# Optimization experiments

Measured on AMD Instinct MI355X. Metric: run time of the kernel, lower is better.

Reference implementation:

```python
import jax, jax.numpy as jnp
import numpy as np

N_NODES = 100000
N_EDGES = 800000
DIM = 128
BN_EPS = 1e-5


def setup_inputs() -> dict:
    key = jax.random.key(0)
    k1, k2, k3 = jax.random.split(key, 3)
    x = jax.random.normal(k1, (N_NODES, DIM), dtype=jnp.float32)
    edge_index = jax.random.randint(k2, (2, N_EDGES), 0, N_NODES, dtype=jnp.int64)
    # xavier-uniform-like init for the linear weight [out, in]
    limit = float(np.sqrt(6.0 / (DIM + DIM)))
    W = jax.random.uniform(k3, (DIM, DIM), dtype=jnp.float32, minval=-limit, maxval=limit)
    bias = jnp.zeros((DIM,), dtype=jnp.float32)
    bn_gamma = jnp.ones((DIM,), dtype=jnp.float32)
    bn_beta = jnp.zeros((DIM,), dtype=jnp.float32)
    return {"x": x, "edge_index": edge_index, "W": W, "bias": bias,
            "bn_gamma": bn_gamma, "bn_beta": bn_beta, "bit_sum": 0}


def reference(x, edge_index, W, bias, bn_gamma, bn_beta, bit_sum):
    n = x.shape[0]
    # Linear (no bias), is_q=False path; q_xw treated as identity.
    h = x @ W.T                                   # [N, D]
    row, col = edge_index[0], edge_index[1]
    # symmetric degree normalization: deg computed over destination (col)
    deg = jax.ops.segment_sum(jnp.ones_like(col, dtype=h.dtype), col, num_segments=n)
    deg_inv_sqrt = jnp.where(deg > 0, jax.lax.rsqrt(jnp.maximum(deg, 1.0)), 0.0)
    norm = deg_inv_sqrt[row] * deg_inv_sqrt[col]  # [E]
    # message: norm * x_j (x_j = h[row]), aggregate (add) at col
    msg = norm[:, None] * h[row]                  # [E, D]
    out = jax.ops.segment_sum(msg, col, num_segments=n)  # [N, D]
    out = out + bias
    # BatchNorm1d (training mode: batch stats, biased variance)
    mean = jnp.mean(out, axis=0)
    var = jnp.var(out, axis=0)
    out = (out - mean) * jax.lax.rsqrt(var + BN_EPS) * bn_gamma + bn_beta
    # activation
    out = jax.nn.relu(out)
    # residual (in_dim == out_dim); dropout p=0 -> identity
    out = out + x
    return (out, 0)
```

## Files before the change

### kernel.cpp

```cpp
#include <hip/hip_runtime.h>
#include <cstddef>

#define NN 100000
#define DD 128
#define ND (NN * DD)
#define BN_EPS 1e-5f
#define LDA 136
#define NREP 16
#define NBKT 392
#define BSH 8
#define EPB 4096
#define NT ((NN + 63) / 64)

typedef __bf16 bf16_t;
typedef bf16_t bf16x8 __attribute__((ext_vector_type(8)));
typedef float f32x4 __attribute__((ext_vector_type(4)));
typedef unsigned int uint;
typedef unsigned short ushort;


__device__ __forceinline__ ushort f2b(float f) {
    uint u = __builtin_bit_cast(uint, f);
    u += 0x7FFFu + ((u >> 16) & 1u);
    return (ushort)(u >> 16);
}
__device__ __forceinline__ float b2f(uint s) {
    return __builtin_bit_cast(float, s << 16);
}
__device__ __forceinline__ float blo(uint u) {
    return __builtin_bit_cast(float, u << 16);
}
__device__ __forceinline__ float bhi(uint u) {
    return __builtin_bit_cast(float, u & 0xFFFF0000u);
}

__device__ __forceinline__ int detect_i64(const int* __restrict__ ei) {
    __shared__ int sflag;
    int t = threadIdx.x;
    if (t < 64) {
        int hi = ei[2 * t + 1];
        unsigned long long b = __ballot(hi == 0);
        if (t == 0) sflag = (b == ~0ull) ? 1 : 0;
    }
    __syncthreads();
    return sflag;
}

__global__ __launch_bounds__(256) void k_prep(const int* __restrict__ ei,
                                              int* __restrict__ bktot, int E, int nbh,
                                              const float* __restrict__ x,
                                              uint* __restrict__ xb,
                                              const float* __restrict__ W,
                                              uint* __restrict__ wb) {
    if ((int)blockIdx.x < nbh) {
        int f = detect_i64(ei);
        __shared__ int hist[NBKT];
        int t = threadIdx.x;
        for (int i = t; i < NBKT; i += 256) hist[i] = 0;
        __syncthreads();
        int base = blockIdx.x * EPB;
        int count = min(EPB, E - base);
        for (int i = t; i < count; i += 256) {
            int e = base + i;
            int c = f ? ei[2 * (E + e)] : ei[E + e];
            atomicAdd(&hist[c >> BSH], 1);
        }
        __syncthreads();
        for (int i = t; i < NBKT; i += 256)
            if (hist[i] > 0) atomicAdd(&bktot[i], hist[i]);
        return;
    }
    int i = (blockIdx.x - nbh) * 256 + threadIdx.x;
    const float* src;
    uint* dst;
    int j;
    if (i < ND / 8) { src = x; dst = xb; j = i; }
    else { j = i - ND / 8; if (j >= (DD * DD) / 8) return; src = W; dst = wb; }
    const float4* s4 = (const float4*)src;
    float4 a = s4[2 * j], b = s4[2 * j + 1];
    uint4 o;
    o.x = (uint)f2b(a.x) | ((uint)f2b(a.y) << 16);
    o.y = (uint)f2b(a.z) | ((uint)f2b(a.w) << 16);
    o.z = (uint)f2b(b.x) | ((uint)f2b(b.y) << 16);
    o.w = (uint)f2b(b.z) | ((uint)f2b(b.w) << 16);
    ((uint4*)dst)[j] = o;
}

__global__ __launch_bounds__(256) void k_bin(const int* __restrict__ ei,
                                             const int* __restrict__ bktot,
                                             int* __restrict__ bcur,
                                             uint2* __restrict__ pairs, int E) {
    int f = detect_i64(ei);
    __shared__ int bb[NBKT], hist[NBKT], scur[NBKT];
    int t = threadIdx.x;
    for (int i = t; i < NBKT; i += 256) { bb[i] = bktot[i]; hist[i] = 0; }
    __syncthreads();
    if (t == 0) {
        int run = 0;
        for (int i = 0; i < NBKT; ++i) { int v = bb[i]; bb[i] = run; run += v; }
    }
    int base = blockIdx.x * EPB;
    int count = min(EPB, E - base);
    int rr[16], cc[16];
#pragma unroll
    for (int k = 0; k < 16; ++k) {
        int i = t + k * 256;
        if (i < count) {
            int e = base + i;
            int r, c;
            if (f) { r = ei[2 * e]; c = ei[2 * (E + e)]; }
            else   { r = ei[e];     c = ei[E + e]; }
            rr[k] = r; cc[k] = c;
            atomicAdd(&hist[c >> BSH], 1);
        }
    }
    __syncthreads();
    for (int i = t; i < NBKT; i += 256)
        if (hist[i] > 0) scur[i] = bb[i] + atomicAdd(&bcur[i], hist[i]);
    __syncthreads();
#pragma unroll
    for (int k = 0; k < 16; ++k) {
        int i = t + k * 256;
        if (i < count) {
            int b = cc[k] >> BSH;
            int pos = atomicAdd(&scur[b], 1);
            pairs[pos] = (uint2){(uint)rr[k], (uint)cc[k]};
        }
    }
}

__global__ __launch_bounds__(256) void k_cnt(const uint2* __restrict__ pairs,
                                             const int* __restrict__ bktot,
                                             int* __restrict__ ptr0,
                                             int* __restrict__ cnt,
                                             float* __restrict__ dinv,
                                             int* __restrict__ srow) {
    __shared__ int sbt[NBKT];
    __shared__ int hist[256], scur[256], ls[256];
    __shared__ int se0, se1;
    int b = blockIdx.x;
    int t = threadIdx.x;
    for (int i = t; i < NBKT; i += 256) sbt[i] = bktot[i];
    hist[t] = 0;
    __syncthreads();
    if (t == 0) {
        int run = 0;
        for (int i = 0; i < b; ++i) run += sbt[i];
        se0 = run; se1 = run + sbt[b];
    }
    __syncthreads();
    int e0 = se0, e1 = se1;
    int nodebase = b << BSH;
    for (int i = e0 + t; i < e1; i += 256)
        atomicAdd(&hist[(int)pairs[i].y - nodebase], 1);
    __syncthreads();
    int c1 = hist[t];
    ls[t] = c1;
    __syncthreads();
    for (int o = 1; o < 256; o <<= 1) {
        int v = (t >= o) ? ls[t - o] : 0;
        __syncthreads();
        ls[t] += v;
        __syncthreads();
    }
    int run = ls[t] - c1 + e0;
    int idx = nodebase + t;
    if (idx < NN) {
        ptr0[idx] = run;
        cnt[idx] = c1;
        dinv[idx] = c1 > 0 ? rsqrtf((float)c1) : 0.f;
    }
    scur[t] = run;
    __syncthreads();
    for (int i = e0 + t; i < e1; i += 256) {
        uint2 p = pairs[i];
        int pos = atomicAdd(&scur[(int)p.y - nodebase], 1);
        srow[pos] = (int)p.x;
    }
}

__global__ __launch_bounds__(512, 4) void k_gg(const uint* __restrict__ xb,
                                               const int* __restrict__ srow,
                                               const int* __restrict__ ptr0,
                                               const int* __restrict__ cnt,
                                               const float* __restrict__ dinv,
                                               const ushort* __restrict__ wb,
                                               ushort* __restrict__ hb,
                                               float* __restrict__ csr,
                                               float* __restrict__ cqr) {
    __shared__ ushort sA[64 * LDA];
    __shared__ float cp[8][64], cq[8][64];
    __shared__ int sS[64], sK[64];
    __shared__ float sD[64];
    __shared__ int qctr;
    int t = threadIdx.x;
    int wave = t >> 6, lane = t & 63;
    int quad = lane >> 4, l16 = lane & 15;
    uint rowbase = (uint)blockIdx.x * 64;

    if (t == 0) qctr = 0;
    if (t < 64) {
        int node = (int)rowbase + t;
        bool v = node < NN;
        sS[t] = v ? ptr0[node] : 0;
        sK[t] = v ? cnt[node] : 0;
        sD[t] = v ? dinv[node] : 0.f;
    }
    __syncthreads();

    for (;;) {
        int nl = 0;
        if (lane == 0) nl = atomicAdd(&qctr, 1);
        int ni = __shfl(nl, 0);
        if (ni >= 64) break;
        int s = sS[ni], k = sK[ni];
        float dc = sD[ni];
        float ax = 0.f, ay = 0.f;
        for (int base = 0; base < k; base += 64) {
            int m = min(k - base, 64);
            int rj = 0; float wj = 0.f;
            if (lane < m) { rj = srow[s + base + lane]; wj = dinv[rj]; }
            int j = 0;
            for (; j + 4 <= m; j += 4) {
                int r0 = __shfl(rj, j);     float w0 = __shfl(wj, j);
                int r1 = __shfl(rj, j + 1); float w1 = __shfl(wj, j + 1);
                int r2 = __shfl(rj, j + 2); float w2 = __shfl(wj, j + 2);
                int r3 = __shfl(rj, j + 3); float w3 = __shfl(wj, j + 3);
                uint v0 = xb[((uint)r0 << 6) + (uint)lane];
                uint v1 = xb[((uint)r1 << 6) + (uint)lane];
                uint v2 = xb[((uint)r2 << 6) + (uint)lane];
                uint v3 = xb[((uint)r3 << 6) + (uint)lane];
                ax = fmaf(w0, blo(v0), ax); ay = fmaf(w0, bhi(v0), ay);
                ax = fmaf(w1, blo(v1), ax); ay = fmaf(w1, bhi(v1), ay);
                ax = fmaf(w2, blo(v2), ax); ay = fmaf(w2, bhi(v2), ay);
                ax = fmaf(w3, blo(v3), ax); ay = fmaf(w3, bhi(v3), ay);
            }
            for (; j < m; ++j) {
                int r = __shfl(rj, j);
                float w = __shfl(wj, j);
                uint v = xb[((uint)r << 6) + (uint)lane];
                ax = fmaf(w, blo(v), ax);
                ay = fmaf(w, bhi(v), ay);
            }
        }
        *(uint*)(sA + ni * LDA + lane * 2) =
            (uint)f2b(dc * ax) | ((uint)f2b(dc * ay) << 16);
    }
    __syncthreads();

    int rg = wave & 3, chh = wave >> 2;
    bf16x8 Af[4];
#pragma unroll
    for (int ks = 0; ks < 4; ++ks)
        Af[ks] = __builtin_bit_cast(
            bf16x8, *(const uint4*)(sA + (rg * 16 + l16) * LDA + ks * 32 + quad * 8));

#pragma unroll
    for (int c = 0; c < 4; ++c) {
        int ctg = chh * 4 + c;
        bf16x8 Bf[4];
#pragma unroll
        for (int ks = 0; ks < 4; ++ks)
            Bf[ks] = __builtin_bit_cast(
                bf16x8,
                *(const uint4*)(wb + (uint)(ctg * 16 + l16) * 128 + ks * 32 + quad * 8));
        f32x4 acc = (f32x4){0.f, 0.f, 0.f, 0.f};
#pragma unroll
        for (int ks = 0; ks < 4; ++ks)
            acc = __builtin_amdgcn_mfma_f32_16x16x32_bf16(Af[ks], Bf[ks], acc, 0, 0, 0);
        float ss = 0.f, qq = 0.f;
#pragma unroll
        for (int r = 0; r < 4; ++r) {
            float v = acc[r];
            ss += v; qq += v * v;
            uint row = rowbase + rg * 16 + quad * 4 + r;
            if (row < NN) hb[row * 128u + (uint)(ctg * 16 + l16)] = f2b(v);
        }
        ss += __shfl_xor(ss, 16); ss += __shfl_xor(ss, 32);
        qq += __shfl_xor(qq, 16); qq += __shfl_xor(qq, 32);
        if (quad == 0) { cp[wave][c * 16 + l16] = ss; cq[wave][c * 16 + l16] = qq; }
    }
    __syncthreads();
    if (t < 128) {
        int w0 = (t >> 6) * 4, lc = t & 63;
        float s = cp[w0][lc] + cp[w0 + 1][lc] + cp[w0 + 2][lc] + cp[w0 + 3][lc];
        float q = cq[w0][lc] + cq[w0 + 1][lc] + cq[w0 + 2][lc] + cq[w0 + 3][lc];
        int rep = ((int)blockIdx.x & (NREP - 1)) * 128 + t;
        atomicAdd(&csr[rep], s);
        atomicAdd(&cqr[rep], q);
    }
}

__global__ __launch_bounds__(256) void k_final(const uint* __restrict__ hb,
                                               const uint* __restrict__ xb,
                                               const float* __restrict__ gamma,
                                               const float* __restrict__ beta,
                                               const float* __restrict__ csr,
                                               const float* __restrict__ cqr,
                                               float* __restrict__ out, int out_size) {
    __shared__ float sa[128], sb[128];
    int t = threadIdx.x;
    const float invN = 1.0f / NN;
    if (t < 128) {
        float s = 0.f;
        for (int i = 0; i < NREP; ++i) s += csr[i * 128 + t];
        sa[t] = s * invN;
    } else {
        int c = t - 128;
        float s = 0.f;
        for (int i = 0; i < NREP; ++i) s += cqr[i * 128 + c];
        sb[c] = s * invN;
    }
    __syncthreads();
    if (t < 128) {
        float m = sa[t];
        float var = sb[t] - m * m;
        float inv = rsqrtf(var + BN_EPS);
        float A = inv * gamma[t];
        float B = beta[t] - m * A;
        sa[t] = A; sb[t] = B;
    }
    __syncthreads();

    int c0 = (t & 7) * 16;
    int u8 = blockIdx.x * 512 + t * 2;
    uint4 hv0 = ((const uint4*)hb)[u8], hv1 = ((const uint4*)hb)[u8 + 1];
    uint4 xv0 = ((const uint4*)xb)[u8], xv1 = ((const uint4*)xb)[u8 + 1];
    uint hu[8] = {hv0.x, hv0.y, hv0.z, hv0.w, hv1.x, hv1.y, hv1.z, hv1.w};
    uint xu[8] = {xv0.x, xv0.y, xv0.z, xv0.w, xv1.x, xv1.y, xv1.z, xv1.w};
    float res[16];
#pragma unroll
    for (int p = 0; p < 8; ++p) {
        int c = c0 + p * 2;
        float h0 = blo(hu[p]), h1 = bhi(hu[p]);
        float x0 = blo(xu[p]), x1 = bhi(xu[p]);
        res[2 * p]     = fmaxf(fmaf(h0, sa[c],     sb[c]),     0.f) + x0;
        res[2 * p + 1] = fmaxf(fmaf(h1, sa[c + 1], sb[c + 1]), 0.f) + x1;
    }
    float4* o4 = (float4*)out;
    int ob = blockIdx.x * 1024 + t * 4;
#pragma unroll
    for (int q = 0; q < 4; ++q)
        o4[ob + q] = (float4){res[4 * q], res[4 * q + 1], res[4 * q + 2], res[4 * q + 3]};
    if (blockIdx.x == 0 && t == 0 && out_size > ND) out[ND] = 0.0f;
}

extern "C" void kernel_launch(void* const* d_in, const int* in_sizes, int n_in,
                              void* d_out, int out_size, void* d_ws, size_t ws_size,
                              hipStream_t stream) {
    const float* x     = (const float*)d_in[0];
    const int*   ei    = (const int*)d_in[1];
    const float* W     = (const float*)d_in[2];
    const float* gamma = (const float*)d_in[4];
    const float* beta  = (const float*)d_in[5];
    float* ws = (float*)d_ws;
    float* out = (float*)d_out;

    uint*   region0  = (uint*)ws;
    uint*   xb       = region0 + ND / 2;
    float*  csr      = (float*)(xb + ND / 2);
    float*  cqr      = csr + NREP * 128;
    int*    bktot    = (int*)(cqr + NREP * 128);
    int*    bcur     = bktot + 512;
    int*    cnt      = bcur + 512;
    int*    ptr0     = cnt + NN;
    float*  dinv     = (float*)(ptr0 + NN);
    int*    srow     = (int*)(dinv + NN);

    int E = in_sizes[1] / 2;
    uint* wb = (uint*)(srow + E);
    uint2* pairs = (uint2*)region0;

    int nbc = (ND / 8 + (DD * DD) / 8 + 255) / 256;
    int nbin = (E + EPB - 1) / EPB;

    hipMemsetAsync(csr, 0, (size_t)(2 * NREP * 128 + 1024) * 4, stream);
    k_prep<<<nbin + nbc, 256, 0, stream>>>(ei, bktot, E, nbin, x, xb, W, wb);
    k_bin<<<nbin, 256, 0, stream>>>(ei, bktot, bcur, pairs, E);
    k_cnt<<<NBKT, 256, 0, stream>>>(pairs, bktot, ptr0, cnt, dinv, srow);
    k_gg<<<NT, 512, 0, stream>>>(xb, srow, ptr0, cnt, dinv, (const ushort*)wb,
                                 (ushort*)region0, csr, cqr);
    k_final<<<ND / 4096, 256, 0, stream>>>(region0, xb, gamma, beta, csr, cqr,
                                           out, out_size);
}
```

Before: 231.8 us.

## Gather four nodes per wave with 16-byte loads and degree-sorted node assignment

The gather phase of the fused aggregate+GEMM kernel is restructured. Each wave now processes four destination nodes at once, one per 16-lane quad, and each lane loads a uint4 (8 bf16 values) instead of a uint. The dynamic atomic work queue is replaced by a static assignment: nodes are ranked by degree so that the four nodes sharing a wave have similar edge counts, which reduces divergence. In exchange, each wave runs to the largest degree in its group with masked weights, and dinv is now fetched per edge by every lane.

Result: faster. 223.2 us (-3.7%).

```diff
diff --git a/kernel.cpp b/kernel.cpp
--- a/kernel.cpp
+++ b/kernel.cpp
@@ -190,15 +190,14 @@
                                                float* __restrict__ cqr) {
     __shared__ ushort sA[64 * LDA];
     __shared__ float cp[8][64], cq[8][64];
-    __shared__ int sS[64], sK[64];
+    __shared__ int sS[64], sK[64], sPerm[64];
     __shared__ float sD[64];
-    __shared__ int qctr;
     int t = threadIdx.x;
     int wave = t >> 6, lane = t & 63;
     int quad = lane >> 4, l16 = lane & 15;
     uint rowbase = (uint)blockIdx.x * 64;
-
-    if (t == 0) qctr = 0;
+    const uint4* xb4 = (const uint4*)xb;
+
     if (t < 64) {
         int node = (int)rowbase + t;
         bool v = node < NN;
@@ -207,44 +206,55 @@
         sD[t] = v ? dinv[node] : 0.f;
     }
     __syncthreads();
-
-    for (;;) {
-        int nl = 0;
-        if (lane == 0) nl = atomicAdd(&qctr, 1);
-        int ni = __shfl(nl, 0);
-        if (ni >= 64) break;
-        int s = sS[ni], k = sK[ni];
-        float dc = sD[ni];
-        float ax = 0.f, ay = 0.f;
-        for (int base = 0; base < k; base += 64) {
-            int m = min(k - base, 64);
-            int rj = 0; float wj = 0.f;
-            if (lane < m) { rj = srow[s + base + lane]; wj = dinv[rj]; }
-            int j = 0;
-            for (; j + 4 <= m; j += 4) {
-                int r0 = __shfl(rj, j);     float w0 = __shfl(wj, j);
-                int r1 = __shfl(rj, j + 1); float w1 = __shfl(wj, j + 1);
-                int r2 = __shfl(rj, j + 2); float w2 = __shfl(wj, j + 2);
-                int r3 = __shfl(rj, j + 3); float w3 = __shfl(wj, j + 3);
-                uint v0 = xb[((uint)r0 << 6) + (uint)lane];
-                uint v1 = xb[((uint)r1 << 6) + (uint)lane];
-                uint v2 = xb[((uint)r2 << 6) + (uint)lane];
-                uint v3 = xb[((uint)r3 << 6) + (uint)lane];
-                ax = fmaf(w0, blo(v0), ax); ay = fmaf(w0, bhi(v0), ay);
-                ax = fmaf(w1, blo(v1), ax); ay = fmaf(w1, bhi(v1), ay);
-                ax = fmaf(w2, blo(v2), ax); ay = fmaf(w2, bhi(v2), ay);
-                ax = fmaf(w3, blo(v3), ax); ay = fmaf(w3, bhi(v3), ay);
+    if (t < 64) {
+        int d = sK[t];
+        int rank = 0;
+#pragma unroll 16
+        for (int j = 0; j < 64; ++j) {
+            int dj = sK[j];
+            rank += (dj > d) || (dj == d && j < t);
+        }
+        sPerm[rank] = t;
+    }
+    __syncthreads();
+
+    for (int bt = 0; bt < 2; ++bt) {
+        int g = bt * 8 + wave;
+        int ni = sPerm[4 * g + quad];
+        int s_here = sS[ni];
+        int k_here = sK[ni];
+        float d_here = sD[ni];
+        int km = sK[sPerm[4 * g]];
+
+        float ax0 = 0.f, ax1 = 0.f, ax2 = 0.f, ax3 = 0.f;
+        float ax4 = 0.f, ax5 = 0.f, ax6 = 0.f, ax7 = 0.f;
+
+        for (int base = 0; base < km; base += 16) {
+            int rem = k_here - base;
+            int rj = 0;
+            if (l16 < rem) rj = srow[s_here + base + l16];
+            int jend = km - base; jend = jend > 16 ? 16 : jend;
+            for (int j = 0; j < jend; j += 4) {
+#pragma unroll
+                for (int u = 0; u < 4; ++u) {
+                    int jj = j + u;
+                    int rsel = __shfl(rj, (lane & 48) + jj);
+                    float w = dinv[rsel];
+                    uint4 v = xb4[((uint)rsel << 4) + (uint)l16];
+                    w = (jj < rem) ? w : 0.f;
+                    ax0 = fmaf(w, blo(v.x), ax0); ax1 = fmaf(w, bhi(v.x), ax1);
+                    ax2 = fmaf(w, blo(v.y), ax2); ax3 = fmaf(w, bhi(v.y), ax3);
+                    ax4 = fmaf(w, blo(v.z), ax4); ax5 = fmaf(w, bhi(v.z), ax5);
+                    ax6 = fmaf(w, blo(v.w), ax6); ax7 = fmaf(w, bhi(v.w), ax7);
+                }
             }
-            for (; j < m; ++j) {
-                int r = __shfl(rj, j);
-                float w = __shfl(wj, j);
-                uint v = xb[((uint)r << 6) + (uint)lane];
-                ax = fmaf(w, blo(v), ax);
-                ay = fmaf(w, bhi(v), ay);
-            }
-        }
-        *(uint*)(sA + ni * LDA + lane * 2) =
-            (uint)f2b(dc * ax) | ((uint)f2b(dc * ay) << 16);
+        }
+        uint4 o;
+        o.x = (uint)f2b(d_here * ax0) | ((uint)f2b(d_here * ax1) << 16);
+        o.y = (uint)f2b(d_here * ax2) | ((uint)f2b(d_here * ax3) << 16);
+        o.z = (uint)f2b(d_here * ax4) | ((uint)f2b(d_here * ax5) << 16);
+        o.w = (uint)f2b(d_here * ax6) | ((uint)f2b(d_here * ax7) << 16);
+        *(uint4*)(sA + ni * LDA + l16 * 8) = o;
     }
     __syncthreads();
 
```
